# Performance work log

Hardware: AMD Instinct MI355X
Metric: run time of the kernel (lower is better)

The kernel has to match this reference:

```python
import jax, jax.numpy as jnp
import numpy as np
from functools import partial

BLUR_K = 5
SIGMA = 1.5
DOWN = 4
SCALE = 5.0
OFFSET = 0.2

_DN = ('NCHW', 'OIHW', 'NCHW')


def _gaussian_kernel(k, sigma):
    x = jnp.arange(k, dtype=jnp.float32) - (k - 1) / 2.0
    g = jnp.exp(-x ** 2 / (2.0 * sigma ** 2))
    g2 = jnp.outer(g, g)
    g2 = g2 / g2.sum()
    return g2.reshape(1, 1, k, k)


def setup_inputs() -> dict:
    key = jax.random.key(0)
    left_rgb = jax.random.uniform(key, (16, 3, 544, 960), dtype=jnp.float32)
    return {"left_rgb": left_rgb}


def reference(left_rgb):
    B, C, H, W = left_rgb.shape
    # rgb -> gray (1x1 conv with fixed weights)
    w = jnp.array([0.2989, 0.587, 0.114], dtype=left_rgb.dtype)
    gray = jnp.einsum('bchw,c->bhw', left_rgb, w)[:, None]  # [B,1,H,W]

    # gaussian blur with reflect padding (torch F.pad mode='reflect')
    pad = BLUR_K // 2
    gray_p = jnp.pad(gray, ((0, 0), (0, 0), (pad, pad), (pad, pad)), mode='reflect')
    gk = _gaussian_kernel(BLUR_K, SIGMA).astype(left_rgb.dtype)
    gray_smooth = jax.lax.conv_general_dilated(gray_p, gk, (1, 1), 'VALID',
                                               dimension_numbers=_DN)

    # sobel gradients (cross-correlation, zero padding=1, same as torch conv2d)
    sx = jnp.array([[-1., 0., 1.], [-2., 0., 2.], [-1., 0., 1.]],
                   dtype=left_rgb.dtype).reshape(1, 1, 3, 3)
    sy = jnp.array([[-1., -2., -1.], [0., 0., 0.], [1., 2., 1.]],
                   dtype=left_rgb.dtype).reshape(1, 1, 3, 3)
    gx = jax.lax.conv_general_dilated(gray_smooth, sx, (1, 1), [(1, 1), (1, 1)],
                                      dimension_numbers=_DN)
    gy = jax.lax.conv_general_dilated(gray_smooth, sy, (1, 1), [(1, 1), (1, 1)],
                                      dimension_numbers=_DN)
    mag = jnp.sqrt(gx ** 2 + gy ** 2 + 1e-6)  # [B,1,H,W]

    # avg_pool2d kernel=stride=DOWN (H, W divisible by DOWN)
    down = mag.reshape(B, 1, H // DOWN, DOWN, W // DOWN, DOWN).mean(axis=(3, 5))

    edge_mask = jax.nn.sigmoid(SCALE * (down - OFFSET)) ** 2.0
    return edge_mask
```

## Files before the change

kernel.cpp:

```cpp
#include <hip/hip_runtime.h>
#include <cmath>

constexpr int B = 16, C = 3, H = 544, W = 960;
constexpr int OH = 136, OW = 240;
constexpr size_t HW = (size_t)H * W;

constexpr int TOH = 8, TOW = 30, NTH = 17, NTW = 8, MH = 32, MW = 120;
constexpr int GR = 40;
constexpr int GS = 132;
constexpr int NT = 5;

__global__ __launch_bounds__(256, 2)
void edge_fused(const float* __restrict__ in, float* __restrict__ out,
                float gn0, float gn1, float gn2)
{
    __shared__ float gray[GR * GS];

    const int tid = threadIdx.x;
    const int blk = blockIdx.x;
    const int tw = blk % NTW;
    const int th = (blk / NTW) % NTH;
    const int b  = blk / (NTW * NTH);
    const int mh0 = th * MH, mw0 = tw * MW;
    const float* inb = in + (size_t)b * C * HW;

    float4 Rv[NT], Gv[NT], Bv[NT];
    #pragma unroll
    for (int k = 0; k < NT; ++k) {
        const int idx = tid + 256 * k;
        const int r = idx >> 5;
        const int c = idx & 31;
        int g = mh0 - 4 + r;
        g = g < 0 ? -g : (g >= H ? 2 * H - 2 - g : g);
        int gcb = mw0 - 4 + 4 * c;
        gcb = gcb < 0 ? 0 : (gcb > W - 4 ? W - 4 : gcb);
        const float* p = inb + (size_t)g * W + gcb;
        Rv[k] = *reinterpret_cast<const float4*>(p);
        Gv[k] = *reinterpret_cast<const float4*>(p + HW);
        Bv[k] = *reinterpret_cast<const float4*>(p + 2 * HW);
    }
    #pragma unroll
    for (int k = 0; k < NT; ++k) {
        const int idx = tid + 256 * k;
        const int r = idx >> 5;
        const int c = idx & 31;
        float4 g;
        g.x = fmaf(0.2989f, Rv[k].x, fmaf(0.587f, Gv[k].x, 0.114f * Bv[k].x));
        g.y = fmaf(0.2989f, Rv[k].y, fmaf(0.587f, Gv[k].y, 0.114f * Bv[k].y));
        g.z = fmaf(0.2989f, Rv[k].z, fmaf(0.587f, Gv[k].z, 0.114f * Bv[k].z));
        g.w = fmaf(0.2989f, Rv[k].w, fmaf(0.587f, Gv[k].w, 0.114f * Bv[k].w));
        const bool edgeq = (tw == 0 && c == 0) || (tw == NTW - 1 && c == 31);
        if (!edgeq)
            *reinterpret_cast<float4*>(&gray[r * GS + 4 * c]) = g;
    }
    if ((tw == 0 || tw == NTW - 1) && tid < GR) {
        const int r = tid;
        const int c = (tw == 0) ? 0 : 31;
        int g = mh0 - 4 + r;
        g = g < 0 ? -g : (g >= H ? 2 * H - 2 - g : g);
        float4 gv;
        float* gp = &gv.x;
        #pragma unroll
        for (int m = 0; m < 4; ++m) {
            int gc = mw0 - 4 + 4 * c + m;
            gc = gc < 0 ? -gc : (gc >= W ? 2 * W - 2 - gc : gc);
            const float* p = inb + (size_t)g * W + gc;
            gp[m] = 0.2989f * p[0] + 0.587f * p[HW] + 0.114f * p[2 * HW];
        }
        *reinterpret_cast<float4*>(&gray[r * GS + 4 * c]) = gv;
    }
    __syncthreads();

    if (tid < TOH * TOW) {
        const int orow = tid / TOW;
        const int ocol = tid - orow * TOW;
        const int lc0 = 4 * ocol;
        const int rb = 4 * orow + 1;

        float sm6[6][6];
        #pragma unroll
        for (int i = 0; i < 6; ++i)
            #pragma unroll
            for (int j = 0; j < 6; ++j) sm6[i][j] = 0.f;

        const float gk[5] = {gn0, gn1, gn2, gn1, gn0};
        #pragma unroll
        for (int tr = 0; tr < 10; ++tr) {
            const float* p = &gray[(rb + tr) * GS + lc0];
            const float4 u = *reinterpret_cast<const float4*>(p);
            const float4 v = *reinterpret_cast<const float4*>(p + 4);
            const float4 w = *reinterpret_cast<const float4*>(p + 8);
            const float t12[12] = {u.x, u.y, u.z, u.w, v.x, v.y, v.z, v.w,
                                   w.x, w.y, w.z, w.w};
            float h6[6];
            #pragma unroll
            for (int j = 0; j < 6; ++j)
                h6[j] = fmaf(gn0, t12[1 + j] + t12[5 + j],
                        fmaf(gn1, t12[2 + j] + t12[4 + j], gn2 * t12[3 + j]));
            #pragma unroll
            for (int i = 0; i < 6; ++i) {
                const int m = tr - i;
                if (m >= 0 && m < 5) {
                    #pragma unroll
                    for (int j = 0; j < 6; ++j)
                        sm6[i][j] = fmaf(gk[m], h6[j], sm6[i][j]);
                }
            }
        }

        #pragma unroll
        for (int i = 0; i < 6; ++i) {
            const int hh = mh0 + 4 * orow - 1 + i;
            const float rm = (hh >= 0 && hh < H) ? 1.f : 0.f;
            #pragma unroll
            for (int j = 0; j < 6; ++j) {
                const int ww = mw0 + 4 * ocol - 1 + j;
                sm6[i][j] *= rm * ((ww >= 0 && ww < W) ? 1.f : 0.f);
            }
        }

        float acc[4] = {0.f, 0.f, 0.f, 0.f};
        #pragma unroll
        for (int i = 0; i < 4; ++i) {
            #pragma unroll
            for (int j = 0; j < 4; ++j) {
                const float a00 = sm6[i][j],     a01 = sm6[i][j + 1],     a02 = sm6[i][j + 2];
                const float a10 = sm6[i + 1][j],                          a12 = sm6[i + 1][j + 2];
                const float a20 = sm6[i + 2][j], a21 = sm6[i + 2][j + 1], a22 = sm6[i + 2][j + 2];
                const float gx = (a02 - a00) + 2.f * (a12 - a10) + (a22 - a20);
                const float gy = (a20 + 2.f * a21 + a22) - (a00 + 2.f * a01 + a02);
                acc[i] += sqrtf(gx * gx + gy * gy + 1e-6f);
            }
        }
        const float down = ((acc[0] + acc[1]) + (acc[2] + acc[3])) * (1.f / 16.f);
        const float x = 5.0f * (down - 0.2f);
        const float sg = 1.f / (1.f + __expf(-x));
        const size_t o = ((size_t)b * OH + (th * TOH + orow)) * OW + (tw * TOW + ocol);
        out[o] = sg * sg;
    }
}

extern "C" void kernel_launch(void* const* d_in, const int* in_sizes, int n_in,
                              void* d_out, int out_size, void* d_ws, size_t ws_size,
                              hipStream_t stream) {
    const float* in = (const float*)d_in[0];
    float* out = (float*)d_out;

    const double g0 = std::exp(-4.0 / 4.5);
    const double g1 = std::exp(-1.0 / 4.5);
    const double g2 = 1.0;
    const double S = 2.0 * (g0 + g1) + g2;
    const float gn0 = (float)(g0 / S);
    const float gn1 = (float)(g1 / S);
    const float gn2 = (float)(g2 / S);

    hipLaunchKernelGGL(edge_fused, dim3(B * NTH * NTW), dim3(256), 0, stream,
                       in, out, gn0, gn1, gn2);
}
```

Measured before the change: 33.54 us.

## Process two batch tiles per block, prefetching second tile during first compute

Each block now handles two images (b0 and b0+8) for the same spatial tile, issuing global loads for the second image before computing the first so load latency overlaps with the blur/sobel compute. The column reflect-padding at image edges is now built by mirroring values already in shared memory instead of a separate scalar global gather, and sqrtf is replaced with a raw v_sqrt_f32. The grid is halved and the launch-bounds occupancy hint is removed, which raises register pressure from holding prefetched data alongside phase-B state and may reduce occupancy.

Result: slower. 38.29 us (+14.2%).

```diff
diff --git a/kernel.cpp b/kernel.cpp
--- a/kernel.cpp
+++ b/kernel.cpp
@@ -1,7 +1,7 @@
 #include <hip/hip_runtime.h>
 #include <cmath>
 
-constexpr int B = 16, C = 3, H = 544, W = 960;
+constexpr int BN = 16, H = 544, W = 960;
 constexpr int OH = 136, OW = 240;
 constexpr size_t HW = (size_t)H * W;
 
@@ -9,8 +9,10 @@
 constexpr int GR = 40;
 constexpr int GS = 132;
 constexpr int NT = 5;
+constexpr int NTILE = BN * NTH * NTW;
+constexpr int GRID = NTILE / 2;
 
-__global__ __launch_bounds__(256, 2)
+__global__ __launch_bounds__(256)
 void edge_fused(const float* __restrict__ in, float* __restrict__ out,
                 float gn0, float gn1, float gn2)
 {
@@ -18,126 +20,147 @@
 
     const int tid = threadIdx.x;
     const int blk = blockIdx.x;
-    const int tw = blk % NTW;
-    const int th = (blk / NTW) % NTH;
-    const int b  = blk / (NTW * NTH);
+    const int tw = blk & 7;
+    const int th = (blk >> 3) % NTH;
+    const int b0 = blk / (NTH * NTW);
     const int mh0 = th * MH, mw0 = tw * MW;
-    const float* inb = in + (size_t)b * C * HW;
+    const float* inb0 = in + (size_t)b0 * 3 * HW;
 
     float4 Rv[NT], Gv[NT], Bv[NT];
-    #pragma unroll
-    for (int k = 0; k < NT; ++k) {
-        const int idx = tid + 256 * k;
-        const int r = idx >> 5;
-        const int c = idx & 31;
-        int g = mh0 - 4 + r;
-        g = g < 0 ? -g : (g >= H ? 2 * H - 2 - g : g);
-        int gcb = mw0 - 4 + 4 * c;
-        gcb = gcb < 0 ? 0 : (gcb > W - 4 ? W - 4 : gcb);
-        const float* p = inb + (size_t)g * W + gcb;
-        Rv[k] = *reinterpret_cast<const float4*>(p);
-        Gv[k] = *reinterpret_cast<const float4*>(p + HW);
-        Bv[k] = *reinterpret_cast<const float4*>(p + 2 * HW);
-    }
-    #pragma unroll
-    for (int k = 0; k < NT; ++k) {
-        const int idx = tid + 256 * k;
-        const int r = idx >> 5;
-        const int c = idx & 31;
-        float4 g;
-        g.x = fmaf(0.2989f, Rv[k].x, fmaf(0.587f, Gv[k].x, 0.114f * Bv[k].x));
-        g.y = fmaf(0.2989f, Rv[k].y, fmaf(0.587f, Gv[k].y, 0.114f * Bv[k].y));
-        g.z = fmaf(0.2989f, Rv[k].z, fmaf(0.587f, Gv[k].z, 0.114f * Bv[k].z));
-        g.w = fmaf(0.2989f, Rv[k].w, fmaf(0.587f, Gv[k].w, 0.114f * Bv[k].w));
-        const bool edgeq = (tw == 0 && c == 0) || (tw == NTW - 1 && c == 31);
-        if (!edgeq)
+
+    auto issue = [&](const float* inb) {
+        #pragma unroll
+        for (int k = 0; k < NT; ++k) {
+            const int idx = tid + 256 * k;
+            const int r = idx >> 5, c = idx & 31;
+            int g = mh0 - 4 + r;
+            g = g < 0 ? -g : (g >= H ? 2 * H - 2 - g : g);
+            int gcb = mw0 - 4 + 4 * c;
+            gcb = gcb < 0 ? 0 : (gcb > W - 4 ? W - 4 : gcb);
+            const float* p = inb + (size_t)g * W + gcb;
+            Rv[k] = *reinterpret_cast<const float4*>(p);
+            Gv[k] = *reinterpret_cast<const float4*>(p + HW);
+            Bv[k] = *reinterpret_cast<const float4*>(p + 2 * HW);
+        }
+        asm volatile("" ::: "memory");
+    };
+
+    auto convert = [&]() {
+        #pragma unroll
+        for (int k = 0; k < NT; ++k) {
+            const int idx = tid + 256 * k;
+            const int r = idx >> 5, c = idx & 31;
+            float4 g;
+            g.x = fmaf(0.2989f, Rv[k].x, fmaf(0.587f, Gv[k].x, 0.114f * Bv[k].x));
+            g.y = fmaf(0.2989f, Rv[k].y, fmaf(0.587f, Gv[k].y, 0.114f * Bv[k].y));
+            g.z = fmaf(0.2989f, Rv[k].z, fmaf(0.587f, Gv[k].z, 0.114f * Bv[k].z));
+            g.w = fmaf(0.2989f, Rv[k].w, fmaf(0.587f, Gv[k].w, 0.114f * Bv[k].w));
             *reinterpret_cast<float4*>(&gray[r * GS + 4 * c]) = g;
-    }
-    if ((tw == 0 || tw == NTW - 1) && tid < GR) {
-        const int r = tid;
-        const int c = (tw == 0) ? 0 : 31;
-        int g = mh0 - 4 + r;
-        g = g < 0 ? -g : (g >= H ? 2 * H - 2 - g : g);
-        float4 gv;
-        float* gp = &gv.x;
-        #pragma unroll
-        for (int m = 0; m < 4; ++m) {
-            int gc = mw0 - 4 + 4 * c + m;
-            gc = gc < 0 ? -gc : (gc >= W ? 2 * W - 2 - gc : gc);
-            const float* p = inb + (size_t)g * W + gc;
-            gp[m] = 0.2989f * p[0] + 0.587f * p[HW] + 0.114f * p[2 * HW];
         }
-        *reinterpret_cast<float4*>(&gray[r * GS + 4 * c]) = gv;
-    }
-    __syncthreads();
-
-    if (tid < TOH * TOW) {
-        const int orow = tid / TOW;
-        const int ocol = tid - orow * TOW;
-        const int lc0 = 4 * ocol;
-        const int rb = 4 * orow + 1;
-
-        float sm6[6][6];
-        #pragma unroll
-        for (int i = 0; i < 6; ++i)
-            #pragma unroll
-            for (int j = 0; j < 6; ++j) sm6[i][j] = 0.f;
-
-        const float gk[5] = {gn0, gn1, gn2, gn1, gn0};
-        #pragma unroll
-        for (int tr = 0; tr < 10; ++tr) {
-            const float* p = &gray[(rb + tr) * GS + lc0];
-            const float4 u = *reinterpret_cast<const float4*>(p);
-            const float4 v = *reinterpret_cast<const float4*>(p + 4);
-            const float4 w = *reinterpret_cast<const float4*>(p + 8);
-            const float t12[12] = {u.x, u.y, u.z, u.w, v.x, v.y, v.z, v.w,
-                                   w.x, w.y, w.z, w.w};
-            float h6[6];
-            #pragma unroll
-            for (int j = 0; j < 6; ++j)
-                h6[j] = fmaf(gn0, t12[1 + j] + t12[5 + j],
-                        fmaf(gn1, t12[2 + j] + t12[4 + j], gn2 * t12[3 + j]));
-            #pragma unroll
-            for (int i = 0; i < 6; ++i) {
-                const int m = tr - i;
-                if (m >= 0 && m < 5) {
-                    #pragma unroll
-                    for (int j = 0; j < 6; ++j)
-                        sm6[i][j] = fmaf(gk[m], h6[j], sm6[i][j]);
+        if (tw == 0 || tw == NTW - 1) {
+            asm volatile("s_waitcnt lgkmcnt(0)" ::: "memory");
+            __builtin_amdgcn_sched_barrier(0);
+            const int l5 = tid & 31;
+            if ((tw == 0 && l5 == 0) || (tw == NTW - 1 && l5 == 31)) {
+                const int base  = (tw == 0) ? 0 : 124;
+                const int sbase = (tw == 0) ? 5 : 119;
+                #pragma unroll
+                for (int k = 0; k < NT; ++k) {
+                    const int r = (tid >> 5) + 8 * k;
+                    float* g = &gray[r * GS];
+                    float4 v;
+                    v.x = g[sbase + 3]; v.y = g[sbase + 2];
+                    v.z = g[sbase + 1]; v.w = g[sbase + 0];
+                    *reinterpret_cast<float4*>(&g[base]) = v;
                 }
             }
         }
+    };
 
-        #pragma unroll
-        for (int i = 0; i < 6; ++i) {
-            const int hh = mh0 + 4 * orow - 1 + i;
-            const float rm = (hh >= 0 && hh < H) ? 1.f : 0.f;
+    auto phaseB = [&](float* outb) {
+        if (tid < TOH * TOW) {
+            const int orow = tid / TOW;
+            const int ocol = tid - orow * TOW;
+            const int lc0 = 4 * ocol;
+            const int rb = 4 * orow + 1;
+
+            float sm6[6][6];
             #pragma unroll
-            for (int j = 0; j < 6; ++j) {
-                const int ww = mw0 + 4 * ocol - 1 + j;
-                sm6[i][j] *= rm * ((ww >= 0 && ww < W) ? 1.f : 0.f);
+            for (int i = 0; i < 6; ++i)
+                #pragma unroll
+                for (int j = 0; j < 6; ++j) sm6[i][j] = 0.f;
+
+            const float gk[5] = {gn0, gn1, gn2, gn1, gn0};
+            #pragma unroll
+            for (int tr = 0; tr < 10; ++tr) {
+                const float* p = &gray[(rb + tr) * GS + lc0];
+                const float4 u = *reinterpret_cast<const float4*>(p);
+                const float4 v = *reinterpret_cast<const float4*>(p + 4);
+                const float4 w = *reinterpret_cast<const float4*>(p + 8);
+                const float t12[12] = {u.x, u.y, u.z, u.w, v.x, v.y, v.z, v.w,
+                                       w.x, w.y, w.z, w.w};
+                float h6[6];
+                #pragma unroll
+                for (int j = 0; j < 6; ++j)
+                    h6[j] = fmaf(gn0, t12[1 + j] + t12[5 + j],
+                            fmaf(gn1, t12[2 + j] + t12[4 + j], gn2 * t12[3 + j]));
+                #pragma unroll
+                for (int i = 0; i < 6; ++i) {
+                    const int m = tr - i;
+                    if (m >= 0 && m < 5) {
+                        #pragma unroll
+                        for (int j = 0; j < 6; ++j)
+                            sm6[i][j] = fmaf(gk[m], h6[j], sm6[i][j]);
+                    }
+                }
             }
+
+            #pragma unroll
+            for (int i = 0; i < 6; ++i) {
+                const int hh = mh0 + 4 * orow - 1 + i;
+                const float rm = (hh >= 0 && hh < H) ? 1.f : 0.f;
+                #pragma unroll
+                for (int j = 0; j < 6; ++j) {
+                    const int ww = mw0 + 4 * ocol - 1 + j;
+                    sm6[i][j] *= rm * ((ww >= 0 && ww < W) ? 1.f : 0.f);
+                }
+            }
+
+            float acc[4] = {0.f, 0.f, 0.f, 0.f};
+            #pragma unroll
+            for (int i = 0; i < 4; ++i) {
+                #pragma unroll
+                for (int j = 0; j < 4; ++j) {
+                    const float a00 = sm6[i][j],     a01 = sm6[i][j + 1],     a02 = sm6[i][j + 2];
+                    const float a10 = sm6[i + 1][j],                          a12 = sm6[i + 1][j + 2];
+                    const float a20 = sm6[i + 2][j], a21 = sm6[i + 2][j + 1], a22 = sm6[i + 2][j + 2];
+                    const float gx = (a02 - a00) + 2.f * (a12 - a10) + (a22 - a20);
+                    const float gy = (a20 + 2.f * a21 + a22) - (a00 + 2.f * a01 + a02);
+                    const float m2 = gx * gx + gy * gy + 1e-6f;
+                    float mg;
+                    asm("v_sqrt_f32 %0, %1" : "=v"(mg) : "v"(m2));
+                    acc[i] += mg;
+                }
+            }
+            const float down = ((acc[0] + acc[1]) + (acc[2] + acc[3])) * (1.f / 16.f);
+            const float x = 5.0f * (down - 0.2f);
+            const float sg = 1.f / (1.f + __expf(-x));
+            outb[(size_t)(mh0 / 4 + orow) * OW + (mw0 / 4 + ocol)] = sg * sg;
         }
+    };
 
-        float acc[4] = {0.f, 0.f, 0.f, 0.f};
-        #pragma unroll
-        for (int i = 0; i < 4; ++i) {
-            #pragma unroll
-            for (int j = 0; j < 4; ++j) {
-                const float a00 = sm6[i][j],     a01 = sm6[i][j + 1],     a02 = sm6[i][j + 2];
-                const float a10 = sm6[i + 1][j],                          a12 = sm6[i + 1][j + 2];
-                const float a20 = sm6[i + 2][j], a21 = sm6[i + 2][j + 1], a22 = sm6[i + 2][j + 2];
-                const float gx = (a02 - a00) + 2.f * (a12 - a10) + (a22 - a20);
-                const float gy = (a20 + 2.f * a21 + a22) - (a00 + 2.f * a01 + a02);
-                acc[i] += sqrtf(gx * gx + gy * gy + 1e-6f);
-            }
-        }
-        const float down = ((acc[0] + acc[1]) + (acc[2] + acc[3])) * (1.f / 16.f);
-        const float x = 5.0f * (down - 0.2f);
-        const float sg = 1.f / (1.f + __expf(-x));
-        const size_t o = ((size_t)b * OH + (th * TOH + orow)) * OW + (tw * TOW + ocol);
-        out[o] = sg * sg;
-    }
+    issue(inb0);
+    convert();
+    __syncthreads();
+
+    issue(inb0 + (size_t)8 * 3 * HW);
+    phaseB(out + (size_t)b0 * OH * OW);
+    __syncthreads();
+
+    convert();
+    __syncthreads();
+
+    phaseB(out + (size_t)(b0 + 8) * OH * OW);
 }
 
 extern "C" void kernel_launch(void* const* d_in, const int* in_sizes, int n_in,
@@ -154,6 +177,6 @@
     const float gn1 = (float)(g1 / S);
     const float gn2 = (float)(g2 / S);
 
-    hipLaunchKernelGGL(edge_fused, dim3(B * NTH * NTW), dim3(256), 0, stream,
+    hipLaunchKernelGGL(edge_fused, dim3(GRID), dim3(256), 0, stream,
                        in, out, gn0, gn1, gn2);
 }
```
